# Performance work log

Hardware: AMD Instinct MI355X
Metric: run time of the kernel (lower is better)

## Reference

```python
import jax, jax.numpy as jnp
import numpy as np

B, T = 256, 400
N_MELS = 80
INPUT_DIMS = 512
DEC = 128
LSTM = 1024
PRENET = 2 * DEC  # 256
FILTERS, KSIZE = 32, 31
MAX_R, R = 20, 1


def setup_inputs() -> dict:
    key = jax.random.key(0)
    ks = iter(jax.random.split(key, 48))
    def act(shape):
        return jax.random.normal(next(ks), shape, dtype=jnp.float32)
    def p(shape):  # small-scale params keep tanh/sigmoid in linear-ish range
        return jax.random.normal(next(ks), shape, dtype=jnp.float32) * 0.02
    return {
        "encoder_seq": act((B, T, INPUT_DIMS)),
        "encoder_seq_proj": act((B, T, DEC)),
        "prenet_in": act((B, N_MELS)),
        "attn_hidden": act((B, DEC)),
        "rnn1_hidden": act((B, LSTM)),
        "rnn2_hidden": act((B, LSTM)),
        "rnn1_cell": act((B, LSTM)),
        "rnn2_cell": act((B, LSTM)),
        "context_vec": act((B, INPUT_DIMS)),
        "cumulative": jax.random.uniform(next(ks), (B, T), dtype=jnp.float32),
        "chars": jax.random.randint(next(ks), (B, T), 0, 60),
        # PreNet
        "prenet_w1": p((PRENET, N_MELS)), "prenet_b1": p((PRENET,)),
        "prenet_w2": p((PRENET, PRENET)), "prenet_b2": p((PRENET,)),
        # attn GRUCell (in = INPUT_DIMS + PRENET)
        "gru_w_ih": p((3 * DEC, INPUT_DIMS + PRENET)), "gru_w_hh": p((3 * DEC, DEC)),
        "gru_b_ih": p((3 * DEC,)), "gru_b_hh": p((3 * DEC,)),
        # LSA attention
        "lsa_conv_w": p((FILTERS, 1, KSIZE)), "lsa_conv_b": p((FILTERS,)),
        "lsa_L": p((DEC, FILTERS)), "lsa_W": p((DEC, DEC)), "lsa_Wb": p((DEC,)),
        "lsa_v": p((1, DEC)),
        # rnn_input Linear (in = INPUT_DIMS + DEC)
        "rnn_in_w": p((LSTM, INPUT_DIMS + DEC)), "rnn_in_b": p((LSTM,)),
        # two LSTMCells
        "lstm1_w_ih": p((4 * LSTM, LSTM)), "lstm1_w_hh": p((4 * LSTM, LSTM)),
        "lstm1_b_ih": p((4 * LSTM,)), "lstm1_b_hh": p((4 * LSTM,)),
        "lstm2_w_ih": p((4 * LSTM, LSTM)), "lstm2_w_hh": p((4 * LSTM, LSTM)),
        "lstm2_b_ih": p((4 * LSTM,)), "lstm2_b_hh": p((4 * LSTM,)),
        # projections
        "mel_w": p((N_MELS * MAX_R, LSTM)),
        "stop_w": p((1, LSTM + INPUT_DIMS)), "stop_b": p((1,)),
    }


def _linear(x, w, b=None):
    y = x @ w.T
    return y + b if b is not None else y


def _gru_cell(x, h, w_ih, w_hh, b_ih, b_hh):
    gi = x @ w_ih.T + b_ih
    gh = h @ w_hh.T + b_hh
    i_r, i_z, i_n = jnp.split(gi, 3, axis=-1)
    h_r, h_z, h_n = jnp.split(gh, 3, axis=-1)
    r = jax.nn.sigmoid(i_r + h_r)
    z = jax.nn.sigmoid(i_z + h_z)
    n = jnp.tanh(i_n + r * h_n)
    return (1.0 - z) * n + z * h


def _lstm_cell(x, h, c, w_ih, w_hh, b_ih, b_hh):
    g = x @ w_ih.T + h @ w_hh.T + (b_ih + b_hh)
    i, f, gg, o = jnp.split(g, 4, axis=-1)
    c_new = jax.nn.sigmoid(f) * c + jax.nn.sigmoid(i) * jnp.tanh(gg)
    h_new = jax.nn.sigmoid(o) * jnp.tanh(c_new)
    return h_new, c_new


def _forward(encoder_seq, encoder_seq_proj, prenet_in, attn_hidden, rnn1_hidden,
             rnn2_hidden, rnn1_cell, rnn2_cell, context_vec, cumulative,
             prenet_w1, prenet_b1, prenet_w2, prenet_b2,
             gru_w_ih, gru_w_hh, gru_b_ih, gru_b_hh,
             lsa_conv_w, lsa_conv_b, lsa_L, lsa_W, lsa_Wb, lsa_v,
             rnn_in_w, rnn_in_b,
             lstm1_w_ih, lstm1_w_hh, lstm1_b_ih, lstm1_b_hh,
             lstm2_w_ih, lstm2_w_hh, lstm2_b_ih, lstm2_b_hh,
             mel_w, stop_w, stop_b, chars):
    # PreNet (eval mode: dropout is identity)
    h = jax.nn.relu(_linear(prenet_in, prenet_w1, prenet_b1))
    prenet_out = jax.nn.relu(_linear(h, prenet_w2, prenet_b2))

    # attention GRU cell
    attn_rnn_in = jnp.concatenate([context_vec, prenet_out], axis=-1)
    attn_hidden = _gru_cell(attn_rnn_in, attn_hidden, gru_w_ih, gru_w_hh, gru_b_ih, gru_b_hh)

    # LSA: location conv over cumulative attention [B,1,T] -> [B,FILTERS,T]
    loc = cumulative[:, None, :]
    conv = jax.lax.conv_general_dilated(
        loc, lsa_conv_w, window_strides=(1,), padding=[((KSIZE - 1) // 2,) * 2],
        dimension_numbers=("NCH", "OIH", "NCH")) + lsa_conv_b[None, :, None]
    processed_loc = jnp.einsum("bft,df->btd", conv, lsa_L)          # [B,T,DEC]
    processed_query = (_linear(attn_hidden, lsa_W, lsa_Wb))[:, None, :]
    u = jnp.einsum("btd,d->bt", jnp.tanh(processed_query + encoder_seq_proj + processed_loc), lsa_v[0])
    u = u * (chars != 0).astype(u.dtype)                             # mask padding chars
    scores_bt = jax.nn.softmax(u, axis=1)                            # [B,T]
    cumulative_new = cumulative + scores_bt
    scores = scores_bt[:, None, :]                                   # [B,1,T]

    # context vector
    context_vec = jnp.einsum("bt,btd->bd", scores_bt, encoder_seq)   # [B,INPUT_DIMS]

    x = jnp.concatenate([context_vec, attn_hidden], axis=1)
    x = _linear(x, rnn_in_w, rnn_in_b)

    rnn1_hidden, rnn1_cell = _lstm_cell(x, rnn1_hidden, rnn1_cell, lstm1_w_ih, lstm1_w_hh, lstm1_b_ih, lstm1_b_hh)
    x = x + rnn1_hidden
    rnn2_hidden, rnn2_cell = _lstm_cell(x, rnn2_hidden, rnn2_cell, lstm2_w_ih, lstm2_w_hh, lstm2_b_ih, lstm2_b_hh)
    x = x + rnn2_hidden

    mels = (x @ mel_w.T).reshape(x.shape[0], N_MELS, MAX_R)[:, :, :R]
    s = jnp.concatenate([x, context_vec], axis=1)
    stop_tokens = jax.nn.sigmoid(_linear(s, stop_w, stop_b))
    return (mels, scores, attn_hidden, rnn1_hidden, rnn2_hidden,
            rnn1_cell, rnn2_cell, context_vec, stop_tokens, cumulative_new)


def reference(encoder_seq, encoder_seq_proj, prenet_in, attn_hidden, rnn1_hidden,
              rnn2_hidden, rnn1_cell, rnn2_cell, context_vec, cumulative, chars,
              prenet_w1, prenet_b1, prenet_w2, prenet_b2,
              gru_w_ih, gru_w_hh, gru_b_ih, gru_b_hh,
              lsa_conv_w, lsa_conv_b, lsa_L, lsa_W, lsa_Wb, lsa_v,
              rnn_in_w, rnn_in_b,
              lstm1_w_ih, lstm1_w_hh, lstm1_b_ih, lstm1_b_hh,
              lstm2_w_ih, lstm2_w_hh, lstm2_b_ih, lstm2_b_hh,
              mel_w, stop_w, stop_b):
    return _forward(encoder_seq, encoder_seq_proj, prenet_in, attn_hidden, rnn1_hidden,
                    rnn2_hidden, rnn1_cell, rnn2_cell, context_vec, cumulative,
                    prenet_w1, prenet_b1, prenet_w2, prenet_b2,
                    gru_w_ih, gru_w_hh, gru_b_ih, gru_b_hh,
                    lsa_conv_w, lsa_conv_b, lsa_L, lsa_W, lsa_Wb, lsa_v,
                    rnn_in_w, rnn_in_b,
                    lstm1_w_ih, lstm1_w_hh, lstm1_b_ih, lstm1_b_hh,
                    lstm2_w_ih, lstm2_w_hh, lstm2_b_ih, lstm2_b_hh,
                    mel_w, stop_w, stop_b, chars)
```

## Files before the change

### kernel.cpp

```cpp
#include <hip/hip_runtime.h>
#include <hip/hip_bf16.h>

#define B_ 256
#define T_ 400
#define NMELS 80
#define INP 512
#define DEC_ 128
#define LSTM_ 1024
#define FILT 32
#define KS 31
#define MAXR 20
#define TCH 2

typedef float f32x4 __attribute__((ext_vector_type(4)));
typedef short bf16x8 __attribute__((ext_vector_type(8)));

__device__ __forceinline__ short f2bf(float f) {
  union { float f; unsigned u; } v; v.f = f;
  unsigned u = v.u;
  unsigned r = (u + 0x7fffu + ((u >> 16) & 1u)) >> 16;
  return (short)r;
}

__device__ __forceinline__ bf16x8 pack8(float4 a0, float4 a1) {
  bf16x8 r;
  r[0] = f2bf(a0.x); r[1] = f2bf(a0.y); r[2] = f2bf(a0.z); r[3] = f2bf(a0.w);
  r[4] = f2bf(a1.x); r[5] = f2bf(a1.y); r[6] = f2bf(a1.z); r[7] = f2bf(a1.w);
  return r;
}

__device__ __forceinline__ float sigmoidf_(float x) {
  return 1.f / (1.f + __expf(-x));
}
__device__ __forceinline__ float tanhf_(float x) {
  float e = __expf(2.f * x);
  return 1.f - 2.f / (e + 1.f);
}

struct Args {
  const float *enc, *esp, *prein, *ah0, *h1_0, *h2_0, *c1_0, *c2_0, *ctx0, *cum;
  const int* chars;
  const float *pw1, *pb1, *pw2, *pb2;
  const float *gwih, *gwhh, *gbih, *gbhh;
  const float *cvw, *cvb, *lsaL, *lsaW, *lsaWb, *lsav;
  const float *riw, *rib;
  const float *l1wih, *l1whh, *l1bih, *l1bhh;
  const float *l2wih, *l2whh, *l2bih, *l2bhh;
  const float *melw, *stopw, *stopb;
  float *o_mels, *o_scores, *o_attn, *o_h1, *o_h2, *o_c1, *o_c2, *o_ctx, *o_stop, *o_cum;
  float *ws_pq, *ws_u, *ws_part, *ws_x, *ws_x2, *ws_g4;
};

__global__ __launch_bounds__(256) void head_kernel(Args a) {
  __shared__ float s_x[768];
  __shared__ float s_p[80];
  __shared__ float s_h1[256];
  __shared__ float s_hold[DEC_];
  __shared__ float s_gi[384];
  __shared__ float s_gh[384];
  __shared__ float s_h2[DEC_];
  const int b = blockIdx.x, tid = threadIdx.x;

  if (tid < 80)   s_p[tid]   = a.prein[(size_t)b * 80 + tid];
  if (tid < DEC_) s_hold[tid] = a.ah0[(size_t)b * DEC_ + tid];
  for (int i = tid; i < INP; i += 256) s_x[i] = a.ctx0[(size_t)b * INP + i];
  __syncthreads();

  {
    const float* w = a.pw1 + (size_t)tid * 80;
    float acc = a.pb1[tid];
#pragma unroll
    for (int k = 0; k < 80; k += 4)
      acc += w[k] * s_p[k] + w[k+1] * s_p[k+1] + w[k+2] * s_p[k+2] + w[k+3] * s_p[k+3];
    s_h1[tid] = fmaxf(acc, 0.f);
  }
  __syncthreads();

  {
    const float4* w = (const float4*)(a.pw2 + (size_t)tid * 256);
    float acc = a.pb2[tid];
#pragma unroll 8
    for (int q = 0; q < 64; ++q) {
      float4 wv = w[q];
      acc += wv.x * s_h1[q*4] + wv.y * s_h1[q*4+1] + wv.z * s_h1[q*4+2] + wv.w * s_h1[q*4+3];
    }
    s_x[INP + tid] = fmaxf(acc, 0.f);
  }
  __syncthreads();

  for (int n = tid; n < 384; n += 256) {
    const float4* w = (const float4*)(a.gwih + (size_t)n * 768);
    float acc = a.gbih[n];
#pragma unroll 8
    for (int q = 0; q < 192; ++q) {
      float4 wv = w[q];
      acc += wv.x * s_x[q*4] + wv.y * s_x[q*4+1] + wv.z * s_x[q*4+2] + wv.w * s_x[q*4+3];
    }
    s_gi[n] = acc;
  }
  for (int n = tid; n < 384; n += 256) {
    const float4* w = (const float4*)(a.gwhh + (size_t)n * DEC_);
    float acc = a.gbhh[n];
#pragma unroll
    for (int q = 0; q < 32; ++q) {
      float4 wv = w[q];
      acc += wv.x * s_hold[q*4] + wv.y * s_hold[q*4+1] + wv.z * s_hold[q*4+2] + wv.w * s_hold[q*4+3];
    }
    s_gh[n] = acc;
  }
  __syncthreads();

  if (tid < DEC_) {
    float r = sigmoidf_(s_gi[tid] + s_gh[tid]);
    float z = sigmoidf_(s_gi[128 + tid] + s_gh[128 + tid]);
    float n = tanhf_(s_gi[256 + tid] + r * s_gh[256 + tid]);
    float h = (1.f - z) * n + z * s_hold[tid];
    s_h2[tid] = h;
    a.o_attn[(size_t)b * DEC_ + tid] = h;
  }
  __syncthreads();

  if (tid < DEC_) {
    const float4* w = (const float4*)(a.lsaW + (size_t)tid * DEC_);
    float acc = a.lsaWb[tid];
#pragma unroll
    for (int q = 0; q < 32; ++q) {
      float4 wv = w[q];
      acc += wv.x * s_h2[q*4] + wv.y * s_h2[q*4+1] + wv.z * s_h2[q*4+2] + wv.w * s_h2[q*4+3];
    }
    a.ws_pq[(size_t)b * DEC_ + tid] = acc;
  }
}

__global__ __launch_bounds__(256) void attn_score_kernel(Args a) {
  __shared__ float s_cum[232];
  __shared__ __align__(16) short s_conv[208][40];
  __shared__ __align__(16) short s_L[128][40];
  __shared__ float s_w[FILT * KS];
  __shared__ float s_cb[FILT];
  __shared__ float s_pq[DEC_];
  __shared__ float s_v[DEC_];

  const int half = blockIdx.x;
  const int b    = blockIdx.y;
  const int tid  = threadIdx.x;
  const int t0   = half * 200;

  for (int i = tid; i < 230; i += 256) {
    int t = t0 - 15 + i;
    s_cum[i] = (t >= 0 && t < T_) ? a.cum[(size_t)b * T_ + t] : 0.f;
  }
  for (int i = tid; i < FILT * KS; i += 256) s_w[i] = a.cvw[i];
  for (int i = tid; i < DEC_ * FILT; i += 256) s_L[i >> 5][i & 31] = f2bf(a.lsaL[i]);
  if (tid < FILT) s_cb[tid] = a.cvb[tid];
  if (tid < DEC_) { s_pq[tid] = a.ws_pq[(size_t)b * DEC_ + tid]; s_v[tid] = a.lsav[tid]; }
  s_conv[200 + (tid >> 5)][tid & 31] = 0;
  __syncthreads();

  if (tid < 200) {
    float c[KS];
#pragma unroll
    for (int k = 0; k < KS; ++k) c[k] = s_cum[tid + k];
#pragma unroll
    for (int f = 0; f < FILT; ++f) {
      float acc = s_cb[f];
#pragma unroll
      for (int k = 0; k < KS; ++k) acc += c[k] * s_w[f * KS + k];
      s_conv[tid][f] = f2bf(acc);
    }
  }
  __syncthreads();

  const int lane = tid & 63, wave = tid >> 6;
  const int l15 = lane & 15, kq = (lane >> 4) * 8;
  for (int m = wave; m < 13; m += 4) {
    bf16x8 af = *(const bf16x8*)&s_conv[m * 16 + l15][kq];
    f32x4 acc[8];
#pragma unroll
    for (int n = 0; n < 8; ++n) {
      bf16x8 bf = *(const bf16x8*)&s_L[n * 16 + l15][kq];
      acc[n] = __builtin_amdgcn_mfma_f32_16x16x32_bf16(af, bf, (f32x4){0.f, 0.f, 0.f, 0.f}, 0, 0, 0);
    }
    const int trow = m * 16 + (lane >> 4) * 4;
    float u[4] = {0.f, 0.f, 0.f, 0.f};
#pragma unroll
    for (int n = 0; n < 8; ++n) {
      int d = n * 16 + l15;
      float pqd = s_pq[d], vd = s_v[d];
#pragma unroll
      for (int r = 0; r < 4; ++r) {
        int tl = trow + r;
        if (tl < 200) {
          float x = acc[n][r] + pqd + a.esp[((size_t)b * T_ + t0 + tl) * DEC_ + d];
          u[r] += tanhf_(x) * vd;
        }
      }
    }
#pragma unroll
    for (int r = 0; r < 4; ++r) {
#pragma unroll
      for (int o = 1; o < 16; o <<= 1) u[r] += __shfl_xor(u[r], o);
    }
    if (l15 == 0) {
#pragma unroll
      for (int r = 0; r < 4; ++r) {
        int tl = trow + r;
        if (tl < 200) {
          int t = t0 + tl;
          float uu = u[r];
          if (a.chars[(size_t)b * T_ + t] == 0) uu = 0.f;
          a.ws_u[(size_t)b * T_ + t] = uu;
        }
      }
    }
  }
}

__global__ __launch_bounds__(256) void ctx_smax_part_kernel(Args a) {
  __shared__ float s_u[T_];
  __shared__ float s_red[8];
  const int tc = blockIdx.x, b = blockIdx.y, tid = threadIdx.x;
  const int lane = tid & 63, wave = tid >> 6;

  float mx = -1e30f;
  for (int t = tid; t < T_; t += 256) {
    float v = a.ws_u[(size_t)b * T_ + t];
    s_u[t] = v;
    mx = fmaxf(mx, v);
  }
#pragma unroll
  for (int o = 32; o >= 1; o >>= 1) mx = fmaxf(mx, __shfl_xor(mx, o));
  if (lane == 0) s_red[wave] = mx;
  __syncthreads();
  mx = fmaxf(fmaxf(s_red[0], s_red[1]), fmaxf(s_red[2], s_red[3]));

  float smv = 0.f;
  for (int t = tid; t < T_; t += 256) {
    float e = __expf(s_u[t] - mx);
    s_u[t] = e;
    smv += e;
  }
#pragma unroll
  for (int o = 32; o >= 1; o >>= 1) smv += __shfl_xor(smv, o);
  if (lane == 0) s_red[4 + wave] = smv;
  __syncthreads();
  smv = s_red[4] + s_red[5] + s_red[6] + s_red[7];
  float inv = 1.f / smv;
  for (int t = tid; t < T_; t += 256) {
    float s = s_u[t] * inv;
    s_u[t] = s;
    if (tc == 0) {
      a.o_scores[(size_t)b * T_ + t] = s;
      a.o_cum[(size_t)b * T_ + t] = a.cum[(size_t)b * T_ + t] + s;
    }
  }
  __syncthreads();

  const int start = tc * 200;
  const float2* Eb = (const float2*)(a.enc + ((size_t)b * T_ + start) * INP) + tid;
  const float* su = &s_u[start];
  float2 a0 = {0.f, 0.f}, a1 = {0.f, 0.f}, a2 = {0.f, 0.f}, a3 = {0.f, 0.f};
  for (int t = 0; t < 200; t += 4) {
    float s0 = su[t], s1 = su[t + 1], s2 = su[t + 2], s3 = su[t + 3];
    float2 e0 = Eb[(size_t)(t)     * 256];
    float2 e1 = Eb[(size_t)(t + 1) * 256];
    float2 e2 = Eb[(size_t)(t + 2) * 256];
    float2 e3 = Eb[(size_t)(t + 3) * 256];
    a0.x += s0 * e0.x; a0.y += s0 * e0.y;
    a1.x += s1 * e1.x; a1.y += s1 * e1.y;
    a2.x += s2 * e2.x; a2.y += s2 * e2.y;
    a3.x += s3 * e3.x; a3.y += s3 * e3.y;
  }
  float2 r;
  r.x = (a0.x + a1.x) + (a2.x + a3.x);
  r.y = (a0.y + a1.y) + (a2.y + a3.y);
  *(float2*)&a.ws_part[((size_t)tc * B_ + b) * INP + 2 * tid] = r;
}

__global__ __launch_bounds__(256) void gemm_bf16(
    const float* __restrict__ A1, const float* __restrict__ A1b,
    float* __restrict__ ctx_side, int lda1,
    const float* __restrict__ W1, int ldw1, int K1,
    const float* __restrict__ A2, int lda2, const float* __restrict__ W2, int ldw2, int K2,
    const float* __restrict__ bias1, const float* __restrict__ bias2,
    float* __restrict__ out, int ldo, int act, int zmode)
{
  __shared__ __align__(16) short sA[64][40];
  __shared__ __align__(16) short sB[64][40];
  const int tid  = threadIdx.x;
  const int lane = tid & 63;
  const int wave = tid >> 6;
  const int wr = (wave >> 1) * 32;
  const int wc = (wave & 1) * 32;
  const int bm = blockIdx.y * 64;
  const int bn = blockIdx.x * 64;
  const int sr = tid >> 2;
  const int sk = (tid & 3) * 8;
  const int l15 = lane & 15;
  const int kq  = (lane >> 4) * 8;

  int kb1 = 0, ke1 = K1, kb2 = 0, ke2 = K2;
  if (zmode == 2) {
    int p = blockIdx.z >> 1, h = blockIdx.z & 1;
    if (p == 0) { ke2 = 0; int half = K1 >> 1; kb1 = h * half; ke1 = kb1 + half; }
    else        { ke1 = 0; int half = K2 >> 1; kb2 = h * half; ke2 = kb2 + half; }
  }
  float* outp = out;
  if (zmode == 2) outp += (size_t)blockIdx.z * (size_t)(gridDim.y * 64) * ldo;

  f32x4 acc[2][2];
#pragma unroll
  for (int i = 0; i < 2; ++i)
#pragma unroll
    for (int j = 0; j < 2; ++j) acc[i][j] = (f32x4){0.f, 0.f, 0.f, 0.f};

  for (int pair = 0; pair < 2; ++pair) {
    const int kb = pair ? kb2 : kb1;
    const int ke = pair ? ke2 : ke1;
    if (ke <= kb) continue;
    const float* A = pair ? A2 : A1;
    const float* Ab = pair ? nullptr : A1b;
    const float* W = pair ? W2 : W1;
    const int lda = pair ? lda2 : lda1;
    const int ldw = pair ? ldw2 : ldw1;
    const float* arow  = A + (size_t)(bm + sr) * lda;
    const float* arowb = Ab ? Ab + (size_t)(bm + sr) * lda : nullptr;
    const float* wrow  = W + (size_t)(bn + sr) * ldw;
    float* crow = (pair == 0 && ctx_side) ? ctx_side + (size_t)(bm + sr) * lda : nullptr;

    float4 ra0, ra1, rb0, rb1;
    if (kb + 32 <= ke) {
      const float* pa = arow + kb + sk;
      const float* pw = wrow + kb + sk;
      ra0 = *(const float4*)pa; ra1 = *(const float4*)(pa + 4);
      if (arowb) {
        const float* pb = arowb + kb + sk;
        float4 b0 = *(const float4*)pb, b1 = *(const float4*)(pb + 4);
        ra0.x += b0.x; ra0.y += b0.y; ra0.z += b0.z; ra0.w += b0.w;
        ra1.x += b1.x; ra1.y += b1.y; ra1.z += b1.z; ra1.w += b1.w;
      }
      rb0 = *(const float4*)pw; rb1 = *(const float4*)(pw + 4);
    }
    for (int k0 = kb; k0 < ke; k0 += 32) {
      __syncthreads();
      if (k0 + 32 <= ke) {
        *(bf16x8*)&sA[sr][sk] = pack8(ra0, ra1);
        *(bf16x8*)&sB[sr][sk] = pack8(rb0, rb1);
        if (crow) {
          *(float4*)(crow + k0 + sk) = ra0;
          *(float4*)(crow + k0 + sk + 4) = ra1;
        }
        if (k0 + 64 <= ke) {
          const float* pa = arow + k0 + 32 + sk;
          const float* pw = wrow + k0 + 32 + sk;
          ra0 = *(const float4*)pa; ra1 = *(const float4*)(pa + 4);
          if (arowb) {
            const float* pb = arowb + k0 + 32 + sk;
            float4 b0 = *(const float4*)pb, b1 = *(const float4*)(pb + 4);
            ra0.x += b0.x; ra0.y += b0.y; ra0.z += b0.z; ra0.w += b0.w;
            ra1.x += b1.x; ra1.y += b1.y; ra1.z += b1.z; ra1.w += b1.w;
          }
          rb0 = *(const float4*)pw; rb1 = *(const float4*)(pw + 4);
        }
      } else {
        short* da = &sA[sr][sk];
        short* db = &sB[sr][sk];
#pragma unroll
        for (int j = 0; j < 8; ++j) {
          int k = k0 + sk + j;
          float av = (k < ke) ? arow[k] + (arowb ? arowb[k] : 0.f) : 0.f;
          da[j] = (k < ke) ? f2bf(av) : (short)0;
          db[j] = (k < ke) ? f2bf(wrow[k]) : (short)0;
        }
      }
      __syncthreads();
      bf16x8 af[2], bfv[2];
      af[0]  = *(const bf16x8*)&sA[wr + l15][kq];
      af[1]  = *(const bf16x8*)&sA[wr + 16 + l15][kq];
      bfv[0] = *(const bf16x8*)&sB[wc + l15][kq];
      bfv[1] = *(const bf16x8*)&sB[wc + 16 + l15][kq];
#pragma unroll
      for (int i = 0; i < 2; ++i)
#pragma unroll
        for (int j = 0; j < 2; ++j)
          acc[i][j] = __builtin_amdgcn_mfma_f32_16x16x32_bf16(af[i], bfv[j], acc[i][j], 0, 0, 0);
    }
  }

#pragma unroll
  for (int i = 0; i < 2; ++i) {
#pragma unroll
    for (int j = 0; j < 2; ++j) {
      int n = bn + wc + j * 16 + l15;
      float bv = 0.f;
      if (zmode == 0) bv = (bias1 ? bias1[n] : 0.f) + (bias2 ? bias2[n] : 0.f);
#pragma unroll
      for (int r = 0; r < 4; ++r) {
        int m = bm + wr + i * 16 + (lane >> 4) * 4 + r;
        float v = acc[i][j][r] + bv;
        if (act == 1) v = fmaxf(v, 0.f);
        outp[(size_t)m * ldo + n] = v;
      }
    }
  }
}

__global__ __launch_bounds__(256) void lstm_cell_kernel(
    const float* __restrict__ g4, const float* __restrict__ bih,
    const float* __restrict__ bhh, const float* __restrict__ c_old,
    const float* __restrict__ x_in,
    float* __restrict__ h_out, float* __restrict__ c_out,
    float* __restrict__ x_out)
{
  const size_t SEG = (size_t)B_ * 4096;
  int idx = blockIdx.x * 256 + threadIdx.x;
  if (idx >= B_ * LSTM_) return;
  int b = idx >> 10, j = idx & 1023;
  const float* gb = g4 + (size_t)b * 4096;
  float ig = gb[j]        + gb[SEG + j]        + gb[2*SEG + j]        + gb[3*SEG + j]        + bih[j]        + bhh[j];
  float fg = gb[1024 + j] + gb[SEG + 1024 + j] + gb[2*SEG + 1024 + j] + gb[3*SEG + 1024 + j] + bih[1024 + j] + bhh[1024 + j];
  float gg = gb[2048 + j] + gb[SEG + 2048 + j] + gb[2*SEG + 2048 + j] + gb[3*SEG + 2048 + j] + bih[2048 + j] + bhh[2048 + j];
  float og = gb[3072 + j] + gb[SEG + 3072 + j] + gb[2*SEG + 3072 + j] + gb[3*SEG + 3072 + j] + bih[3072 + j] + bhh[3072 + j];
  float cn = sigmoidf_(fg) * c_old[idx] + sigmoidf_(ig) * tanhf_(gg);
  float hn = sigmoidf_(og) * tanhf_(cn);
  h_out[idx] = hn;
  c_out[idx] = cn;
  x_out[idx] = x_in[idx] + hn;
}

__global__ __launch_bounds__(256) void mel_stop_kernel(Args a) {
  __shared__ float s_x[LSTM_];
  __shared__ float s_c[INP];
  __shared__ float s_red[4];
  const int part = blockIdx.x;
  const int b    = blockIdx.y;
  const int tid  = threadIdx.x;
  const int lane = tid & 63, wave = tid >> 6;

  for (int k = tid * 4; k < LSTM_; k += 1024)
    *(float4*)&s_x[k] = *(const float4*)&a.ws_x[(size_t)b * LSTM_ + k];
  if (part == 0)
    for (int k = tid; k < INP; k += 256) s_c[k] = a.o_ctx[(size_t)b * INP + k];
  __syncthreads();

  const int n0 = part * 20 + wave * 5;
  const float* w0 = a.melw + (size_t)(n0)     * MAXR * LSTM_;
  const float* w1 = a.melw + (size_t)(n0 + 1) * MAXR * LSTM_;
  const float* w2 = a.melw + (size_t)(n0 + 2) * MAXR * LSTM_;
  const float* w3 = a.melw + (size_t)(n0 + 3) * MAXR * LSTM_;
  const float* w4 = a.melw + (size_t)(n0 + 4) * MAXR * LSTM_;
  float ac0 = 0.f, ac1 = 0.f, ac2 = 0.f, ac3 = 0.f, ac4 = 0.f;
#pragma unroll
  for (int j = 0; j < 4; ++j) {
    int k = j * 256 + lane * 4;
    float4 xv = *(const float4*)&s_x[k];
    float4 v0 = *(const float4*)(w0 + k);
    float4 v1 = *(const float4*)(w1 + k);
    float4 v2 = *(const float4*)(w2 + k);
    float4 v3 = *(const float4*)(w3 + k);
    float4 v4 = *(const float4*)(w4 + k);
    ac0 += v0.x * xv.x + v0.y * xv.y + v0.z * xv.z + v0.w * xv.w;
    ac1 += v1.x * xv.x + v1.y * xv.y + v1.z * xv.z + v1.w * xv.w;
    ac2 += v2.x * xv.x + v2.y * xv.y + v2.z * xv.z + v2.w * xv.w;
    ac3 += v3.x * xv.x + v3.y * xv.y + v3.z * xv.z + v3.w * xv.w;
    ac4 += v4.x * xv.x + v4.y * xv.y + v4.z * xv.z + v4.w * xv.w;
  }
#pragma unroll
  for (int o = 32; o >= 1; o >>= 1) {
    ac0 += __shfl_xor(ac0, o);
    ac1 += __shfl_xor(ac1, o);
    ac2 += __shfl_xor(ac2, o);
    ac3 += __shfl_xor(ac3, o);
    ac4 += __shfl_xor(ac4, o);
  }
  if (lane == 0) {
    float* om = a.o_mels + (size_t)b * NMELS + n0;
    om[0] = ac0; om[1] = ac1; om[2] = ac2; om[3] = ac3; om[4] = ac4;
  }

  if (part == 0) {
    float p = 0.f;
    for (int k = tid; k < LSTM_; k += 256) p += s_x[k] * a.stopw[k];
    for (int k = tid; k < INP; k += 256) p += s_c[k] * a.stopw[LSTM_ + k];
#pragma unroll
    for (int o = 32; o >= 1; o >>= 1) p += __shfl_xor(p, o);
    if (lane == 0) s_red[wave] = p;
    __syncthreads();
    if (tid == 0) {
      float t = s_red[0] + s_red[1] + s_red[2] + s_red[3] + a.stopb[0];
      a.o_stop[b] = sigmoidf_(t);
    }
  }
}

extern "C" void kernel_launch(void* const* d_in, const int* in_sizes, int n_in,
                              void* d_out, int out_size, void* d_ws, size_t ws_size,
                              hipStream_t stream) {
  Args a;
  a.enc   = (const float*)d_in[0];
  a.esp   = (const float*)d_in[1];
  a.prein = (const float*)d_in[2];
  a.ah0   = (const float*)d_in[3];
  a.h1_0  = (const float*)d_in[4];
  a.h2_0  = (const float*)d_in[5];
  a.c1_0  = (const float*)d_in[6];
  a.c2_0  = (const float*)d_in[7];
  a.ctx0  = (const float*)d_in[8];
  a.cum   = (const float*)d_in[9];
  a.chars = (const int*)d_in[10];
  a.pw1 = (const float*)d_in[11];  a.pb1 = (const float*)d_in[12];
  a.pw2 = (const float*)d_in[13];  a.pb2 = (const float*)d_in[14];
  a.gwih = (const float*)d_in[15]; a.gwhh = (const float*)d_in[16];
  a.gbih = (const float*)d_in[17]; a.gbhh = (const float*)d_in[18];
  a.cvw = (const float*)d_in[19];  a.cvb = (const float*)d_in[20];
  a.lsaL = (const float*)d_in[21]; a.lsaW = (const float*)d_in[22];
  a.lsaWb = (const float*)d_in[23]; a.lsav = (const float*)d_in[24];
  a.riw = (const float*)d_in[25];  a.rib = (const float*)d_in[26];
  a.l1wih = (const float*)d_in[27]; a.l1whh = (const float*)d_in[28];
  a.l1bih = (const float*)d_in[29]; a.l1bhh = (const float*)d_in[30];
  a.l2wih = (const float*)d_in[31]; a.l2whh = (const float*)d_in[32];
  a.l2bih = (const float*)d_in[33]; a.l2bhh = (const float*)d_in[34];
  a.melw = (const float*)d_in[35]; a.stopw = (const float*)d_in[36];
  a.stopb = (const float*)d_in[37];

  float* out = (float*)d_out;
  a.o_mels   = out;
  a.o_scores = out + 20480;
  a.o_attn   = out + 122880;
  a.o_h1     = out + 155648;
  a.o_h2     = out + 417792;
  a.o_c1     = out + 679936;
  a.o_c2     = out + 942080;
  a.o_ctx    = out + 1204224;
  a.o_stop   = out + 1335296;
  a.o_cum    = out + 1335552;

  float* ws = (float*)d_ws;
  a.ws_pq   = ws;
  a.ws_u    = ws + 32768;
  a.ws_part = ws + 135168;
  a.ws_x    = ws + 397312;
  a.ws_x2   = ws + 659456;
  a.ws_g4   = ws + 921600;

  dim3 blk(256);

  head_kernel<<<dim3(B_), blk, 0, stream>>>(a);
  attn_score_kernel<<<dim3(2, B_), blk, 0, stream>>>(a);
  ctx_smax_part_kernel<<<dim3(TCH, B_), blk, 0, stream>>>(a);
  gemm_bf16<<<dim3(16, 4, 1), blk, 0, stream>>>(
      a.ws_part, a.ws_part + (size_t)B_ * INP, a.o_ctx, 512,
      a.riw, 640, 512,
      a.o_attn, 128, a.riw + 512, 640, 128,
      a.rib, nullptr, a.ws_x, 1024, 0, 0);
  gemm_bf16<<<dim3(64, 4, 4), blk, 0, stream>>>(
      a.ws_x, nullptr, nullptr, 1024, a.l1wih, 1024, 1024,
      a.h1_0, 1024, a.l1whh, 1024, 1024,
      nullptr, nullptr, a.ws_g4, 4096, 0, 2);
  lstm_cell_kernel<<<dim3(1024), blk, 0, stream>>>(
      a.ws_g4, a.l1bih, a.l1bhh, a.c1_0, a.ws_x, a.o_h1, a.o_c1, a.ws_x2);
  gemm_bf16<<<dim3(64, 4, 4), blk, 0, stream>>>(
      a.ws_x2, nullptr, nullptr, 1024, a.l2wih, 1024, 1024,
      a.h2_0, 1024, a.l2whh, 1024, 1024,
      nullptr, nullptr, a.ws_g4, 4096, 0, 2);
  lstm_cell_kernel<<<dim3(1024), blk, 0, stream>>>(
      a.ws_g4, a.l2bih, a.l2bhh, a.c2_0, a.ws_x2, a.o_h2, a.o_c2, a.ws_x);
  mel_stop_kernel<<<dim3(4, B_), blk, 0, stream>>>(a);
}
```

Before: 271.1 us.

## Fuse head into attention-score kernel and second LSTM cell into mel projection

Result: slower. 310.0 us (+14.3%).

```diff
diff --git a/kernel.cpp b/kernel.cpp
--- a/kernel.cpp
+++ b/kernel.cpp
@@ -48,22 +48,47 @@
   const float *l2wih, *l2whh, *l2bih, *l2bhh;
   const float *melw, *stopw, *stopb;
   float *o_mels, *o_scores, *o_attn, *o_h1, *o_h2, *o_c1, *o_c2, *o_ctx, *o_stop, *o_cum;
-  float *ws_pq, *ws_u, *ws_part, *ws_x, *ws_x2, *ws_g4;
+  float *ws_u, *ws_part, *ws_x, *ws_x2, *ws_g4;
 };
 
-__global__ __launch_bounds__(256) void head_kernel(Args a) {
-  __shared__ float s_x[768];
-  __shared__ float s_p[80];
-  __shared__ float s_h1[256];
-  __shared__ float s_hold[DEC_];
-  __shared__ float s_gi[384];
-  __shared__ float s_gh[384];
-  __shared__ float s_h2[DEC_];
-  const int b = blockIdx.x, tid = threadIdx.x;
-
-  if (tid < 80)   s_p[tid]   = a.prein[(size_t)b * 80 + tid];
-  if (tid < DEC_) s_hold[tid] = a.ah0[(size_t)b * DEC_ + tid];
-  for (int i = tid; i < INP; i += 256) s_x[i] = a.ctx0[(size_t)b * INP + i];
+struct HeadOv {
+  float s_p[80];
+  float s_hold[DEC_];
+  float s_h1[256];
+  float s_x[768];
+  float s_gi[384];
+  float s_gh[384];
+};
+struct ConvOv {
+  short s_conv[208][40];
+  short s_L[128][40];
+};
+
+__global__ __launch_bounds__(256) void attn_fused_kernel(Args a) {
+  __shared__ float s_cum[232];
+  __shared__ float s_w[FILT * KS];
+  __shared__ float s_cb[FILT];
+  __shared__ float s_pq[DEC_];
+  __shared__ float s_v[DEC_];
+  __shared__ __align__(16) char ovl[sizeof(ConvOv)];
+  HeadOv* H = (HeadOv*)ovl;
+  ConvOv* C = (ConvOv*)ovl;
+
+  const int half = blockIdx.x;
+  const int b    = blockIdx.y;
+  const int tid  = threadIdx.x;
+  const int t0   = half * 200;
+
+  for (int i = tid; i < 230; i += 256) {
+    int t = t0 - 15 + i;
+    s_cum[i] = (t >= 0 && t < T_) ? a.cum[(size_t)b * T_ + t] : 0.f;
+  }
+  for (int i = tid; i < FILT * KS; i += 256) s_w[i] = a.cvw[i];
+  if (tid < FILT) s_cb[tid] = a.cvb[tid];
+  if (tid < DEC_) s_v[tid] = a.lsav[tid];
+  if (tid < 80)   H->s_p[tid]    = a.prein[(size_t)b * 80 + tid];
+  if (tid >= 128 && tid < 256) H->s_hold[tid - 128] = a.ah0[(size_t)b * DEC_ + tid - 128];
+  for (int i = tid; i < INP; i += 256) H->s_x[i] = a.ctx0[(size_t)b * INP + i];
   __syncthreads();
 
   {
@@ -71,32 +96,30 @@
     float acc = a.pb1[tid];
 #pragma unroll
     for (int k = 0; k < 80; k += 4)
-      acc += w[k] * s_p[k] + w[k+1] * s_p[k+1] + w[k+2] * s_p[k+2] + w[k+3] * s_p[k+3];
-    s_h1[tid] = fmaxf(acc, 0.f);
-  }
-  __syncthreads();
-
+      acc += w[k] * H->s_p[k] + w[k+1] * H->s_p[k+1] + w[k+2] * H->s_p[k+2] + w[k+3] * H->s_p[k+3];
+    H->s_h1[tid] = fmaxf(acc, 0.f);
+  }
+  __syncthreads();
   {
     const float4* w = (const float4*)(a.pw2 + (size_t)tid * 256);
     float acc = a.pb2[tid];
 #pragma unroll 8
     for (int q = 0; q < 64; ++q) {
       float4 wv = w[q];
-      acc += wv.x * s_h1[q*4] + wv.y * s_h1[q*4+1] + wv.z * s_h1[q*4+2] + wv.w * s_h1[q*4+3];
-    }
-    s_x[INP + tid] = fmaxf(acc, 0.f);
-  }
-  __syncthreads();
-
+      acc += wv.x * H->s_h1[q*4] + wv.y * H->s_h1[q*4+1] + wv.z * H->s_h1[q*4+2] + wv.w * H->s_h1[q*4+3];
+    }
+    H->s_x[INP + tid] = fmaxf(acc, 0.f);
+  }
+  __syncthreads();
   for (int n = tid; n < 384; n += 256) {
     const float4* w = (const float4*)(a.gwih + (size_t)n * 768);
     float acc = a.gbih[n];
 #pragma unroll 8
     for (int q = 0; q < 192; ++q) {
       float4 wv = w[q];
-      acc += wv.x * s_x[q*4] + wv.y * s_x[q*4+1] + wv.z * s_x[q*4+2] + wv.w * s_x[q*4+3];
-    }
-    s_gi[n] = acc;
+      acc += wv.x * H->s_x[q*4] + wv.y * H->s_x[q*4+1] + wv.z * H->s_x[q*4+2] + wv.w * H->s_x[q*4+3];
+    }
+    H->s_gi[n] = acc;
   }
   for (int n = tid; n < 384; n += 256) {
     const float4* w = (const float4*)(a.gwhh + (size_t)n * DEC_);
@@ -104,57 +127,34 @@
 #pragma unroll
     for (int q = 0; q < 32; ++q) {
       float4 wv = w[q];
-      acc += wv.x * s_hold[q*4] + wv.y * s_hold[q*4+1] + wv.z * s_hold[q*4+2] + wv.w * s_hold[q*4+3];
-    }
-    s_gh[n] = acc;
-  }
-  __syncthreads();
-
+      acc += wv.x * H->s_hold[q*4] + wv.y * H->s_hold[q*4+1] + wv.z * H->s_hold[q*4+2] + wv.w * H->s_hold[q*4+3];
+    }
+    H->s_gh[n] = acc;
+  }
+  __syncthreads();
   if (tid < DEC_) {
-    float r = sigmoidf_(s_gi[tid] + s_gh[tid]);
-    float z = sigmoidf_(s_gi[128 + tid] + s_gh[128 + tid]);
-    float n = tanhf_(s_gi[256 + tid] + r * s_gh[256 + tid]);
-    float h = (1.f - z) * n + z * s_hold[tid];
-    s_h2[tid] = h;
-    a.o_attn[(size_t)b * DEC_ + tid] = h;
-  }
-  __syncthreads();
-
+    float r = sigmoidf_(H->s_gi[tid] + H->s_gh[tid]);
+    float z = sigmoidf_(H->s_gi[128 + tid] + H->s_gh[128 + tid]);
+    float n = tanhf_(H->s_gi[256 + tid] + r * H->s_gh[256 + tid]);
+    float h = (1.f - z) * n + z * H->s_hold[tid];
+    H->s_hold[tid] = h;
+    if (half == 0) a.o_attn[(size_t)b * DEC_ + tid] = h;
+  }
+  __syncthreads();
   if (tid < DEC_) {
     const float4* w = (const float4*)(a.lsaW + (size_t)tid * DEC_);
     float acc = a.lsaWb[tid];
 #pragma unroll
     for (int q = 0; q < 32; ++q) {
       float4 wv = w[q];
-      acc += wv.x * s_h2[q*4] + wv.y * s_h2[q*4+1] + wv.z * s_h2[q*4+2] + wv.w * s_h2[q*4+3];
-    }
-    a.ws_pq[(size_t)b * DEC_ + tid] = acc;
-  }
-}
-
-__global__ __launch_bounds__(256) void attn_score_kernel(Args a) {
-  __shared__ float s_cum[232];
-  __shared__ __align__(16) short s_conv[208][40];
-  __shared__ __align__(16) short s_L[128][40];
-  __shared__ float s_w[FILT * KS];
-  __shared__ float s_cb[FILT];
-  __shared__ float s_pq[DEC_];
-  __shared__ float s_v[DEC_];
-
-  const int half = blockIdx.x;
-  const int b    = blockIdx.y;
-  const int tid  = threadIdx.x;
-  const int t0   = half * 200;
-
-  for (int i = tid; i < 230; i += 256) {
-    int t = t0 - 15 + i;
-    s_cum[i] = (t >= 0 && t < T_) ? a.cum[(size_t)b * T_ + t] : 0.f;
-  }
-  for (int i = tid; i < FILT * KS; i += 256) s_w[i] = a.cvw[i];
-  for (int i = tid; i < DEC_ * FILT; i += 256) s_L[i >> 5][i & 31] = f2bf(a.lsaL[i]);
-  if (tid < FILT) s_cb[tid] = a.cvb[tid];
-  if (tid < DEC_) { s_pq[tid] = a.ws_pq[(size_t)b * DEC_ + tid]; s_v[tid] = a.lsav[tid]; }
-  s_conv[200 + (tid >> 5)][tid & 31] = 0;
+      acc += wv.x * H->s_hold[q*4] + wv.y * H->s_hold[q*4+1] + wv.z * H->s_hold[q*4+2] + wv.w * H->s_hold[q*4+3];
+    }
+    s_pq[tid] = acc;
+  }
+  __syncthreads();
+
+  for (int i = tid; i < DEC_ * FILT; i += 256) C->s_L[i >> 5][i & 31] = f2bf(a.lsaL[i]);
+  C->s_conv[200 + (tid >> 5)][tid & 31] = 0;
   __syncthreads();
 
   if (tid < 200) {
@@ -166,7 +166,7 @@
       float acc = s_cb[f];
 #pragma unroll
       for (int k = 0; k < KS; ++k) acc += c[k] * s_w[f * KS + k];
-      s_conv[tid][f] = f2bf(acc);
+      C->s_conv[tid][f] = f2bf(acc);
     }
   }
   __syncthreads();
@@ -174,11 +174,11 @@
   const int lane = tid & 63, wave = tid >> 6;
   const int l15 = lane & 15, kq = (lane >> 4) * 8;
   for (int m = wave; m < 13; m += 4) {
-    bf16x8 af = *(const bf16x8*)&s_conv[m * 16 + l15][kq];
+    bf16x8 af = *(const bf16x8*)&C->s_conv[m * 16 + l15][kq];
     f32x4 acc[8];
 #pragma unroll
     for (int n = 0; n < 8; ++n) {
-      bf16x8 bf = *(const bf16x8*)&s_L[n * 16 + l15][kq];
+      bf16x8 bf = *(const bf16x8*)&C->s_L[n * 16 + l15][kq];
       acc[n] = __builtin_amdgcn_mfma_f32_16x16x32_bf16(af, bf, (f32x4){0.f, 0.f, 0.f, 0.f}, 0, 0, 0);
     }
     const int trow = m * 16 + (lane >> 4) * 4;
@@ -428,7 +428,7 @@
   x_out[idx] = x_in[idx] + hn;
 }
 
-__global__ __launch_bounds__(256) void mel_stop_kernel(Args a) {
+__global__ __launch_bounds__(256) void mel_cell_kernel(Args a) {
   __shared__ float s_x[LSTM_];
   __shared__ float s_c[INP];
   __shared__ float s_red[4];
@@ -436,9 +436,20 @@
   const int b    = blockIdx.y;
   const int tid  = threadIdx.x;
   const int lane = tid & 63, wave = tid >> 6;
-
-  for (int k = tid * 4; k < LSTM_; k += 1024)
-    *(float4*)&s_x[k] = *(const float4*)&a.ws_x[(size_t)b * LSTM_ + k];
+  const size_t SEG = (size_t)B_ * 4096;
+
+  const float* gb = a.ws_g4 + (size_t)b * 4096;
+  for (int j = tid; j < LSTM_; j += 256) {
+    float ig = gb[j]        + gb[SEG + j]        + gb[2*SEG + j]        + gb[3*SEG + j]        + a.l2bih[j]        + a.l2bhh[j];
+    float fg = gb[1024 + j] + gb[SEG + 1024 + j] + gb[2*SEG + 1024 + j] + gb[3*SEG + 1024 + j] + a.l2bih[1024 + j] + a.l2bhh[1024 + j];
+    float gg = gb[2048 + j] + gb[SEG + 2048 + j] + gb[2*SEG + 2048 + j] + gb[3*SEG + 2048 + j] + a.l2bih[2048 + j] + a.l2bhh[2048 + j];
+    float og = gb[3072 + j] + gb[SEG + 3072 + j] + gb[2*SEG + 3072 + j] + gb[3*SEG + 3072 + j] + a.l2bih[3072 + j] + a.l2bhh[3072 + j];
+    size_t idx = (size_t)b * LSTM_ + j;
+    float cn = sigmoidf_(fg) * a.c2_0[idx] + sigmoidf_(ig) * tanhf_(gg);
+    float hn = sigmoidf_(og) * tanhf_(cn);
+    if (part == 0) { a.o_h2[idx] = hn; a.o_c2[idx] = cn; }
+    s_x[j] = a.ws_x2[idx] + hn;
+  }
   if (part == 0)
     for (int k = tid; k < INP; k += 256) s_c[k] = a.o_ctx[(size_t)b * INP + k];
   __syncthreads();
@@ -536,17 +547,15 @@
   a.o_cum    = out + 1335552;
 
   float* ws = (float*)d_ws;
-  a.ws_pq   = ws;
-  a.ws_u    = ws + 32768;
-  a.ws_part = ws + 135168;
-  a.ws_x    = ws + 397312;
-  a.ws_x2   = ws + 659456;
-  a.ws_g4   = ws + 921600;
+  a.ws_u    = ws;
+  a.ws_part = ws + 102400;
+  a.ws_x    = ws + 364544;
+  a.ws_x2   = ws + 626688;
+  a.ws_g4   = ws + 888832;
 
   dim3 blk(256);
 
-  head_kernel<<<dim3(B_), blk, 0, stream>>>(a);
-  attn_score_kernel<<<dim3(2, B_), blk, 0, stream>>>(a);
+  attn_fused_kernel<<<dim3(2, B_), blk, 0, stream>>>(a);
   ctx_smax_part_kernel<<<dim3(TCH, B_), blk, 0, stream>>>(a);
   gemm_bf16<<<dim3(16, 4, 1), blk, 0, stream>>>(
       a.ws_part, a.ws_part + (size_t)B_ * INP, a.o_ctx, 512,
@@ -563,7 +572,5 @@
       a.ws_x2, nullptr, nullptr, 1024, a.l2wih, 1024, 1024,
       a.h2_0, 1024, a.l2whh, 1024, 1024,
       nullptr, nullptr, a.ws_g4, 4096, 0, 2);
-  lstm_cell_kernel<<<dim3(1024), blk, 0, stream>>>(
-      a.ws_g4, a.l2bih, a.l2bhh, a.c2_0, a.ws_x2, a.o_h2, a.o_c2, a.ws_x);
-  mel_stop_kernel<<<dim3(4, B_), blk, 0, stream>>>(a);
-}
+  mel_cell_kernel<<<dim3(4, B_), blk, 0, stream>>>(a);
+}
```

## Replace MFMA attention score with per-thread fp32 dot products and split accumulators

Applied to the files above, without the earlier changes.

Measured after the change: 256.7 us. 5.3% less time.

```diff
diff --git a/kernel.cpp b/kernel.cpp
--- a/kernel.cpp
+++ b/kernel.cpp
@@ -78,25 +78,27 @@
 
   {
     const float4* w = (const float4*)(a.pw2 + (size_t)tid * 256);
-    float acc = a.pb2[tid];
+    float a0 = a.pb2[tid], a1 = 0.f;
 #pragma unroll 8
-    for (int q = 0; q < 64; ++q) {
-      float4 wv = w[q];
-      acc += wv.x * s_h1[q*4] + wv.y * s_h1[q*4+1] + wv.z * s_h1[q*4+2] + wv.w * s_h1[q*4+3];
-    }
-    s_x[INP + tid] = fmaxf(acc, 0.f);
+    for (int q = 0; q < 32; ++q) {
+      float4 w0 = w[q], w1 = w[32 + q];
+      a0 += w0.x * s_h1[q*4]       + w0.y * s_h1[q*4+1]       + w0.z * s_h1[q*4+2]       + w0.w * s_h1[q*4+3];
+      a1 += w1.x * s_h1[128 + q*4] + w1.y * s_h1[128 + q*4+1] + w1.z * s_h1[128 + q*4+2] + w1.w * s_h1[128 + q*4+3];
+    }
+    s_x[INP + tid] = fmaxf(a0 + a1, 0.f);
   }
   __syncthreads();
 
   for (int n = tid; n < 384; n += 256) {
     const float4* w = (const float4*)(a.gwih + (size_t)n * 768);
-    float acc = a.gbih[n];
+    float a0 = a.gbih[n], a1 = 0.f;
 #pragma unroll 8
-    for (int q = 0; q < 192; ++q) {
-      float4 wv = w[q];
-      acc += wv.x * s_x[q*4] + wv.y * s_x[q*4+1] + wv.z * s_x[q*4+2] + wv.w * s_x[q*4+3];
-    }
-    s_gi[n] = acc;
+    for (int q = 0; q < 96; ++q) {
+      float4 w0 = w[q], w1 = w[96 + q];
+      a0 += w0.x * s_x[q*4]       + w0.y * s_x[q*4+1]       + w0.z * s_x[q*4+2]       + w0.w * s_x[q*4+3];
+      a1 += w1.x * s_x[384 + q*4] + w1.y * s_x[384 + q*4+1] + w1.z * s_x[384 + q*4+2] + w1.w * s_x[384 + q*4+3];
+    }
+    s_gi[n] = a0 + a1;
   }
   for (int n = tid; n < 384; n += 256) {
     const float4* w = (const float4*)(a.gwhh + (size_t)n * DEC_);
@@ -134,10 +136,9 @@
 
 __global__ __launch_bounds__(256) void attn_score_kernel(Args a) {
   __shared__ float s_cum[232];
-  __shared__ __align__(16) short s_conv[208][40];
-  __shared__ __align__(16) short s_L[128][40];
   __shared__ float s_w[FILT * KS];
   __shared__ float s_cb[FILT];
+  __shared__ float s_L[DEC_ * FILT];
   __shared__ float s_pq[DEC_];
   __shared__ float s_v[DEC_];
 
@@ -151,13 +152,16 @@
     s_cum[i] = (t >= 0 && t < T_) ? a.cum[(size_t)b * T_ + t] : 0.f;
   }
   for (int i = tid; i < FILT * KS; i += 256) s_w[i] = a.cvw[i];
-  for (int i = tid; i < DEC_ * FILT; i += 256) s_L[i >> 5][i & 31] = f2bf(a.lsaL[i]);
+  for (int i = tid; i < DEC_ * FILT; i += 256) s_L[i] = a.lsaL[i];
   if (tid < FILT) s_cb[tid] = a.cvb[tid];
   if (tid < DEC_) { s_pq[tid] = a.ws_pq[(size_t)b * DEC_ + tid]; s_v[tid] = a.lsav[tid]; }
-  s_conv[200 + (tid >> 5)][tid & 31] = 0;
-  __syncthreads();
-
-  if (tid < 200) {
+  __syncthreads();
+
+  if (tid >= 200) return;
+  const int t = t0 + tid;
+
+  float cf[FILT];
+  {
     float c[KS];
 #pragma unroll
     for (int k = 0; k < KS; ++k) c[k] = s_cum[tid + k];
@@ -166,54 +170,39 @@
       float acc = s_cb[f];
 #pragma unroll
       for (int k = 0; k < KS; ++k) acc += c[k] * s_w[f * KS + k];
-      s_conv[tid][f] = f2bf(acc);
-    }
-  }
-  __syncthreads();
-
-  const int lane = tid & 63, wave = tid >> 6;
-  const int l15 = lane & 15, kq = (lane >> 4) * 8;
-  for (int m = wave; m < 13; m += 4) {
-    bf16x8 af = *(const bf16x8*)&s_conv[m * 16 + l15][kq];
-    f32x4 acc[8];
-#pragma unroll
-    for (int n = 0; n < 8; ++n) {
-      bf16x8 bf = *(const bf16x8*)&s_L[n * 16 + l15][kq];
-      acc[n] = __builtin_amdgcn_mfma_f32_16x16x32_bf16(af, bf, (f32x4){0.f, 0.f, 0.f, 0.f}, 0, 0, 0);
-    }
-    const int trow = m * 16 + (lane >> 4) * 4;
-    float u[4] = {0.f, 0.f, 0.f, 0.f};
-#pragma unroll
-    for (int n = 0; n < 8; ++n) {
-      int d = n * 16 + l15;
-      float pqd = s_pq[d], vd = s_v[d];
-#pragma unroll
-      for (int r = 0; r < 4; ++r) {
-        int tl = trow + r;
-        if (tl < 200) {
-          float x = acc[n][r] + pqd + a.esp[((size_t)b * T_ + t0 + tl) * DEC_ + d];
-          u[r] += tanhf_(x) * vd;
-        }
-      }
-    }
-#pragma unroll
-    for (int r = 0; r < 4; ++r) {
-#pragma unroll
-      for (int o = 1; o < 16; o <<= 1) u[r] += __shfl_xor(u[r], o);
-    }
-    if (l15 == 0) {
-#pragma unroll
-      for (int r = 0; r < 4; ++r) {
-        int tl = trow + r;
-        if (tl < 200) {
-          int t = t0 + tl;
-          float uu = u[r];
-          if (a.chars[(size_t)b * T_ + t] == 0) uu = 0.f;
-          a.ws_u[(size_t)b * T_ + t] = uu;
-        }
-      }
-    }
-  }
+      cf[f] = acc;
+    }
+  }
+
+  const float4* e4 = (const float4*)(a.esp + ((size_t)b * T_ + t) * DEC_);
+  float u0 = 0.f, u1 = 0.f;
+  for (int d4 = 0; d4 < DEC_ / 4; d4 += 2) {
+    float4 e0 = e4[d4];
+    float4 e1 = e4[d4 + 1];
+    const float ev0[4] = {e0.x, e0.y, e0.z, e0.w};
+    const float ev1[4] = {e1.x, e1.y, e1.z, e1.w};
+#pragma unroll
+    for (int c = 0; c < 4; ++c) {
+      int d = d4 * 4 + c;
+      float pl = 0.f;
+      const float* ld = &s_L[d * FILT];
+#pragma unroll
+      for (int f = 0; f < FILT; ++f) pl += cf[f] * ld[f];
+      u0 += tanhf_(s_pq[d] + ev0[c] + pl) * s_v[d];
+    }
+#pragma unroll
+    for (int c = 0; c < 4; ++c) {
+      int d = (d4 + 1) * 4 + c;
+      float pl = 0.f;
+      const float* ld = &s_L[d * FILT];
+#pragma unroll
+      for (int f = 0; f < FILT; ++f) pl += cf[f] * ld[f];
+      u1 += tanhf_(s_pq[d] + ev1[c] + pl) * s_v[d];
+    }
+  }
+  float u = u0 + u1;
+  if (a.chars[(size_t)b * T_ + t] == 0) u = 0.f;
+  a.ws_u[(size_t)b * T_ + t] = u;
 }
 
 __global__ __launch_bounds__(256) void ctx_smax_part_kernel(Args a) {
```
